# Kernel tuning notes

Hardware: AMD Instinct MI355X
Metric: run time of the kernel (lower is better)

## Reference

```python
import jax, jax.numpy as jnp
import numpy as np

N = 131072      # number of nodes / samples
IN_DIM = 128    # input_dim
H = 128         # hidden_dim
OUT_DIM = 10    # output_dim


def setup_inputs() -> dict:
    key = jax.random.key(0)
    ks = jax.random.split(key, 20)
    s = 0.05
    def rn(k, shape):
        return jax.random.normal(k, shape, jnp.float32) * s
    return {
        "x": jax.random.normal(ks[0], (N, IN_DIM), jnp.float32),
        # GRU layer 1 (seq_len=1, h0=0 => weight_hh contributes nothing; only b_hh matters)
        "w_ih_f1": rn(ks[1], (3 * H, IN_DIM)), "b_ih_f1": rn(ks[2], (3 * H,)), "b_hh_f1": rn(ks[3], (3 * H,)),
        "w_ih_b1": rn(ks[4], (3 * H, IN_DIM)), "b_ih_b1": rn(ks[5], (3 * H,)), "b_hh_b1": rn(ks[6], (3 * H,)),
        # GRU layer 2 (input 2H)
        "w_ih_f2": rn(ks[7], (3 * H, 2 * H)), "b_ih_f2": rn(ks[8], (3 * H,)), "b_hh_f2": rn(ks[9], (3 * H,)),
        "w_ih_b2": rn(ks[10], (3 * H, 2 * H)), "b_ih_b2": rn(ks[11], (3 * H,)), "b_hh_b2": rn(ks[12], (3 * H,)),
        # GCNConv layers
        "w_g1": rn(ks[13], (2 * H, 128)), "b_g1": rn(ks[14], (128,)),
        "w_g2": rn(ks[15], (128, 64)), "b_g2": rn(ks[16], (64,)),
        # final fc
        "w_fc": rn(ks[17], (64, OUT_DIM)), "b_fc": rn(ks[18], (OUT_DIM,)),
    }


def _gru_cell_zero(x, w_ih, b_ih, b_hh):
    # PyTorch GRU cell with h_prev = 0: h' = (1 - z) * n_gate
    gi = x @ w_ih.T + b_ih                    # [n, 3H]
    ir, iz, inn = jnp.split(gi, 3, axis=-1)
    hr, hz, hn = jnp.split(b_hh, 3)
    r = jax.nn.sigmoid(ir + hr)
    z = jax.nn.sigmoid(iz + hz)
    ng = jnp.tanh(inn + r * hn)
    return (1.0 - z) * ng


def _gcn(x, w, b, sources, targets, n):
    # PyG GCNConv: D^{-1/2}(A+I)D^{-1/2} X W + b, self-loops already in edge lists
    xw = x @ w                                 # [n, out]
    deg = jax.ops.segment_sum(jnp.ones(sources.shape[0], x.dtype), targets, num_segments=n)
    dinv = jax.lax.rsqrt(deg)
    norm = dinv[sources] * dinv[targets]       # [E]
    msg = norm[:, None] * xw[sources]          # gather
    return jax.ops.segment_sum(msg, targets, num_segments=n) + b  # scatter-add


def reference(x, w_ih_f1, b_ih_f1, b_hh_f1, w_ih_b1, b_ih_b1, b_hh_b1,
              w_ih_f2, b_ih_f2, b_hh_f2, w_ih_b2, b_ih_b2, b_hh_b2,
              w_g1, b_g1, w_g2, b_g2, w_fc, b_fc):
    n = x.shape[0]
    # seq_len = 1 => bidirectional GRU output is [fwd_cell(x); bwd_cell(x)]
    h1 = jnp.concatenate([_gru_cell_zero(x, w_ih_f1, b_ih_f1, b_hh_f1),
                          _gru_cell_zero(x, w_ih_b1, b_ih_b1, b_hh_b1)], axis=-1)
    h2 = jnp.concatenate([_gru_cell_zero(h1, w_ih_f2, b_ih_f2, b_hh_f2),
                          _gru_cell_zero(h1, w_ih_b2, b_ih_b2, b_hh_b2)], axis=-1)
    # chain graph, both directions, plus self loops (GCNConv adds them)
    src = jnp.arange(n - 1)
    dst = jnp.arange(1, n)
    ar = jnp.arange(n)
    sources = jnp.concatenate([src, dst, ar])
    targets = jnp.concatenate([dst, src, ar])
    g1 = _gcn(h2, w_g1, b_g1, sources, targets, n)   # dropout is identity in eval
    g2 = _gcn(g1, w_g2, b_g2, sources, targets, n)
    return g2 @ w_fc + b_fc
```

## Files before the change

kernel.cpp:

```cpp
#include <hip/hip_runtime.h>
#include <stdint.h>

#define N_NODES 131072
#define HDIM 128

typedef __bf16 bf16x8 __attribute__((ext_vector_type(8)));
typedef float f32x4 __attribute__((ext_vector_type(4)));
typedef unsigned short us8 __attribute__((ext_vector_type(8)));
typedef unsigned short ushort_t;

__device__ __forceinline__ float bf2f(ushort_t u) {
    union { float f; uint32_t i; } v; v.i = ((uint32_t)u) << 16; return v.f;
}
__device__ __forceinline__ ushort_t f2bf(float f) {
    union { float f; uint32_t i; } v; v.f = f;
    uint32_t i = v.i;
    return (ushort_t)((i + 0x7FFFu + ((i >> 16) & 1u)) >> 16);
}

__device__ __forceinline__ void gll16(const ushort_t* g, ushort_t* l) {
    __builtin_amdgcn_global_load_lds(
        (const __attribute__((address_space(1))) uint32_t*)g,
        (__attribute__((address_space(3))) uint32_t*)l, 16, 0, 0);
}

__device__ __forceinline__ bf16x8 ldsw(const ushort_t* base, int R, int g) {
    return *(const bf16x8*)&base[R * 64 + (((g - R) & 7) << 3)];
}

__device__ __forceinline__ float fsig(float x) {
    return __builtin_amdgcn_rcpf(1.0f + __expf(-x));
}
__device__ __forceinline__ float ftanh(float y) {
    float yc = fminf(fmaxf(y, -15.0f), 15.0f);
    float e = __expf(2.0f * yc);
    return (e - 1.0f) * __builtin_amdgcn_rcpf(e + 1.0f);
}

template<int NC>
__device__ __forceinline__ void swz(int b, int& m, int& c) {
    int mhi = b / (8 * NC);
    int rem = b - mhi * (8 * NC);
    c = rem >> 3;
    m = mhi * 8 + (rem & 7);
}

__global__ __launch_bounds__(256) void prep_weights(
    const float* __restrict__ w_f1, const float* __restrict__ w_b1,
    const float* __restrict__ w_f2, const float* __restrict__ w_b2,
    ushort_t* __restrict__ PWF1, ushort_t* __restrict__ PWB1,
    ushort_t* __restrict__ PWF2, ushort_t* __restrict__ PWB2)
{
    int idx = blockIdx.x * 256 + threadIdx.x;
    if (idx < 49152) {
        PWF1[idx] = f2bf(w_f1[idx]);
    } else if (idx < 98304) {
        int j = idx - 49152;  PWB1[j] = f2bf(w_b1[j]);
    } else if (idx < 196608) {
        int j = idx - 98304;  PWF2[j] = f2bf(w_f2[j]);
    } else if (idx < 294912) {
        int j = idx - 196608; PWB2[j] = f2bf(w_b2[j]);
    }
}

__global__ __launch_bounds__(256) void prep_M(
    const float* __restrict__ w_g1, const float* __restrict__ b_g1,
    const float* __restrict__ w_g2, const float* __restrict__ b_g2,
    const float* __restrict__ w_fc, const float* __restrict__ b_fc,
    ushort_t* __restrict__ M16, float* __restrict__ cc)
{
    __shared__ float wfc_s[640];
    __shared__ float T1[128][10];
    const int t = threadIdx.x;
    for (int i = t; i < 640; i += 256) wfc_s[i] = w_fc[i];
    __syncthreads();
    if (t < 128) {
        float s[10];
        #pragma unroll
        for (int j = 0; j < 10; ++j) s[j] = 0.0f;
        const float4* row = (const float4*)(w_g2 + t * 64);
        #pragma unroll
        for (int k4 = 0; k4 < 16; ++k4) {
            float4 v = row[k4];
            #pragma unroll
            for (int j = 0; j < 10; ++j)
                s[j] += v.x * wfc_s[(k4 * 4 + 0) * 10 + j] + v.y * wfc_s[(k4 * 4 + 1) * 10 + j]
                      + v.z * wfc_s[(k4 * 4 + 2) * 10 + j] + v.w * wfc_s[(k4 * 4 + 3) * 10 + j];
        }
        #pragma unroll
        for (int j = 0; j < 10; ++j) T1[t][j] = s[j];
    }
    __syncthreads();
    float m[10];
    #pragma unroll
    for (int j = 0; j < 10; ++j) m[j] = 0.0f;
    const float4* row1 = (const float4*)(w_g1 + t * 128);
    #pragma unroll 4
    for (int k4 = 0; k4 < 32; ++k4) {
        float4 v = row1[k4];
        #pragma unroll
        for (int j = 0; j < 10; ++j)
            m[j] += v.x * T1[k4 * 4 + 0][j] + v.y * T1[k4 * 4 + 1][j]
                  + v.z * T1[k4 * 4 + 2][j] + v.w * T1[k4 * 4 + 3][j];
    }
    #pragma unroll
    for (int j = 0; j < 16; ++j)
        M16[j * 256 + t] = (j < 10) ? f2bf(m[j]) : (ushort_t)0;
    if (t < 10) {
        float s1 = 0.0f;
        for (int k2 = 0; k2 < 128; ++k2) s1 += b_g1[k2] * T1[k2][t];
        cc[t] = s1;
        float s2 = 0.0f;
        for (int k3 = 0; k3 < 64; ++k3) s2 += b_g2[k3] * wfc_s[k3 * 10 + t];
        cc[16 + t] = s2 + b_fc[t];
    }
}

__global__ __launch_bounds__(256, 4) void gru_l1(
    const float* __restrict__ X,
    const ushort_t* __restrict__ Wf,
    const ushort_t* __restrict__ Wb,
    const float* __restrict__ bi_f, const float* __restrict__ bh_f,
    const float* __restrict__ bi_b, const float* __restrict__ bh_b,
    ushort_t* __restrict__ Hout)
{
    __shared__ ushort_t As[128 * 64];
    __shared__ ushort_t Bs[96 * 64];
    const int tid = threadIdx.x;
    int mt, comb;
    swz<8>(blockIdx.x, mt, comb);
    const int m0 = mt * 128;
    const int dir = comb >> 2;
    const int j0 = (comb & 3) * 32;
    const ushort_t* W = dir ? Wb : Wf;
    const float* b_ih = dir ? bi_b : bi_f;
    const float* b_hh = dir ? bh_b : bh_f;
    const int coloff = dir << 7;

    const int wv = tid >> 6, lane = tid & 63;
    const int lr = lane & 15, lq = lane >> 4;
    const int tr = tid >> 3, tc = tid & 7;
    const int sc = ((tr + tc) & 7) << 3;

    f32x4 acc[3][2][2];
    #pragma unroll
    for (int g = 0; g < 3; ++g)
        #pragma unroll
        for (int rt = 0; rt < 2; ++rt)
            #pragma unroll
            for (int ct = 0; ct < 2; ++ct)
                #pragma unroll
                for (int e = 0; e < 4; ++e) acc[g][rt][ct][e] = 0.0f;

    for (int t = 0; t < 2; ++t) {
        const int k0 = t * 64;
        const float* ga = X + (size_t)(m0 + tr) * 128 + k0 + sc;
        float4 fa[4][2];
        #pragma unroll
        for (int i = 0; i < 4; ++i) {
            const float4* p = (const float4*)(ga + (size_t)i * 32 * 128);
            fa[i][0] = p[0]; fa[i][1] = p[1];
        }
        #pragma unroll
        for (int i = 0; i < 3; ++i) {
            int wr = (i << 7) + j0 + tr;
            gll16(W + (size_t)wr * 128 + k0 + sc, &Bs[(i * 256 + tid) * 8]);
        }
        #pragma unroll
        for (int i = 0; i < 4; ++i) {
            us8 t8;
            t8[0] = f2bf(fa[i][0].x); t8[1] = f2bf(fa[i][0].y);
            t8[2] = f2bf(fa[i][0].z); t8[3] = f2bf(fa[i][0].w);
            t8[4] = f2bf(fa[i][1].x); t8[5] = f2bf(fa[i][1].y);
            t8[6] = f2bf(fa[i][1].z); t8[7] = f2bf(fa[i][1].w);
            *(us8*)&As[(i * 256 + tid) * 8] = t8;
        }
        __syncthreads();
        #pragma unroll
        for (int kk = 0; kk < 64; kk += 32) {
            const int g8 = (kk >> 3) + lq;
            bf16x8 a0 = ldsw(As, wv * 32 + lr, g8);
            bf16x8 a1 = ldsw(As, wv * 32 + 16 + lr, g8);
            #pragma unroll
            for (int g = 0; g < 3; ++g) {
                #pragma unroll
                for (int ct = 0; ct < 2; ++ct) {
                    bf16x8 b = ldsw(Bs, g * 32 + ct * 16 + lr, g8);
                    acc[g][0][ct] = __builtin_amdgcn_mfma_f32_16x16x32_bf16(a0, b, acc[g][0][ct], 0, 0, 0);
                    acc[g][1][ct] = __builtin_amdgcn_mfma_f32_16x16x32_bf16(a1, b, acc[g][1][ct], 0, 0, 0);
                }
            }
        }
        __syncthreads();
    }

    #pragma unroll
    for (int ct = 0; ct < 2; ++ct) {
        const int j = j0 + ct * 16 + lr;
        const float br  = b_ih[j] + b_hh[j];
        const float bz  = b_ih[HDIM + j] + b_hh[HDIM + j];
        const float bn  = b_ih[2 * HDIM + j];
        const float bhn = b_hh[2 * HDIM + j];
        #pragma unroll
        for (int rt = 0; rt < 2; ++rt) {
            #pragma unroll
            for (int r = 0; r < 4; ++r) {
                const int row = m0 + wv * 32 + rt * 16 + lq * 4 + r;
                float rg = fsig(acc[0][rt][ct][r] + br);
                float zg = fsig(acc[1][rt][ct][r] + bz);
                float ng = ftanh(acc[2][rt][ct][r] + bn + rg * bhn);
                Hout[(size_t)row * 256 + coloff + j] = f2bf((1.0f - zg) * ng);
            }
        }
    }
}

__global__ __launch_bounds__(256, 5) void gru_l2(
    const ushort_t* __restrict__ A,
    const ushort_t* __restrict__ Wf,
    const ushort_t* __restrict__ Wb,
    const float* __restrict__ bi_f, const float* __restrict__ bh_f,
    const float* __restrict__ bi_b, const float* __restrict__ bh_b,
    const ushort_t* __restrict__ M16,
    float* __restrict__ Zp)
{
    __shared__ ushort_t As[128 * 64];
    __shared__ ushort_t Bs[96 * 64];
    const int tid = threadIdx.x;
    int mt, comb;
    swz<8>(blockIdx.x, mt, comb);
    const int m0 = mt * 128;
    const int dir = comb >> 2;
    const int j0 = (comb & 3) * 32;
    const ushort_t* W = dir ? Wb : Wf;
    const float* b_ih = dir ? bi_b : bi_f;
    const float* b_hh = dir ? bh_b : bh_f;
    const int coloff = dir << 7;

    const int wv = tid >> 6, lane = tid & 63;
    const int lr = lane & 15, lq = lane >> 4;
    const int tr = tid >> 3, tc = tid & 7;
    const int sc = ((tr + tc) & 7) << 3;

    f32x4 acc[3][2][2];
    #pragma unroll
    for (int g = 0; g < 3; ++g)
        #pragma unroll
        for (int rt = 0; rt < 2; ++rt)
            #pragma unroll
            for (int ct = 0; ct < 2; ++ct)
                #pragma unroll
                for (int e = 0; e < 4; ++e) acc[g][rt][ct][e] = 0.0f;

    for (int t = 0; t < 4; ++t) {
        const int k0 = t * 64;
        const ushort_t* ga = A + (size_t)(m0 + tr) * 256 + k0 + sc;
        #pragma unroll
        for (int i = 0; i < 4; ++i)
            gll16(ga + (size_t)i * 32 * 256, &As[(i * 256 + tid) * 8]);
        #pragma unroll
        for (int i = 0; i < 3; ++i) {
            int wr = (i << 7) + j0 + tr;
            gll16(W + (size_t)wr * 256 + k0 + sc, &Bs[(i * 256 + tid) * 8]);
        }
        __syncthreads();
        #pragma unroll
        for (int kk = 0; kk < 64; kk += 32) {
            const int g8 = (kk >> 3) + lq;
            bf16x8 a0 = ldsw(As, wv * 32 + lr, g8);
            bf16x8 a1 = ldsw(As, wv * 32 + 16 + lr, g8);
            #pragma unroll
            for (int g = 0; g < 3; ++g) {
                #pragma unroll
                for (int ct = 0; ct < 2; ++ct) {
                    bf16x8 b = ldsw(Bs, g * 32 + ct * 16 + lr, g8);
                    acc[g][0][ct] = __builtin_amdgcn_mfma_f32_16x16x32_bf16(a0, b, acc[g][0][ct], 0, 0, 0);
                    acc[g][1][ct] = __builtin_amdgcn_mfma_f32_16x16x32_bf16(a1, b, acc[g][1][ct], 0, 0, 0);
                }
            }
        }
        __syncthreads();
    }

    const bf16x8 mb = *(const bf16x8*)&M16[lr * 256 + coloff + j0 + lq * 8];

    ushort_t* hs = &As[wv * 1280];
    #pragma unroll
    for (int ct = 0; ct < 2; ++ct) {
        const int j = j0 + ct * 16 + lr;
        const float br  = b_ih[j] + b_hh[j];
        const float bz  = b_ih[HDIM + j] + b_hh[HDIM + j];
        const float bn  = b_ih[2 * HDIM + j];
        const float bhn = b_hh[2 * HDIM + j];
        #pragma unroll
        for (int rt = 0; rt < 2; ++rt) {
            #pragma unroll
            for (int r = 0; r < 4; ++r) {
                const int lrow = rt * 16 + lq * 4 + r;
                float rg = fsig(acc[0][rt][ct][r] + br);
                float zg = fsig(acc[1][rt][ct][r] + bz);
                float ng = ftanh(acc[2][rt][ct][r] + bn + rg * bhn);
                hs[lrow * 40 + ct * 16 + lr] = f2bf((1.0f - zg) * ng);
            }
        }
    }
    __syncthreads();

    bf16x8 ha0 = *(const bf16x8*)&hs[lr * 40 + lq * 8];
    bf16x8 ha1 = *(const bf16x8*)&hs[(16 + lr) * 40 + lq * 8];
    f32x4 z0, z1;
    #pragma unroll
    for (int e = 0; e < 4; ++e) { z0[e] = 0.0f; z1[e] = 0.0f; }
    z0 = __builtin_amdgcn_mfma_f32_16x16x32_bf16(ha0, mb, z0, 0, 0, 0);
    z1 = __builtin_amdgcn_mfma_f32_16x16x32_bf16(ha1, mb, z1, 0, 0, 0);

    if (lr < 10) {
        float* zslice = Zp + (size_t)comb * (N_NODES * 10);
        #pragma unroll
        for (int r = 0; r < 4; ++r) {
            zslice[(size_t)(m0 + wv * 32 + lq * 4 + r) * 10 + lr] = z0[r];
            zslice[(size_t)(m0 + wv * 32 + 16 + lq * 4 + r) * 10 + lr] = z1[r];
        }
    }
}

__global__ __launch_bounds__(256) void zsum(
    const float4* __restrict__ Zp4, float4* __restrict__ Zc4)
{
    int i = blockIdx.x * 256 + threadIdx.x;
    float4 a = Zp4[i];
    #pragma unroll
    for (int s = 1; s < 8; ++s) {
        float4 b = Zp4[(size_t)s * 327680 + i];
        a.x += b.x; a.y += b.y; a.z += b.z; a.w += b.w;
    }
    Zc4[i] = a;
}

__device__ __forceinline__ float dcoef(int i) {
    return (i == 0 || i == N_NODES - 1) ? 0.70710678118654752f : 0.57735026918962576f;
}
__global__ __launch_bounds__(256) void st5(
    const float* __restrict__ z, float* __restrict__ out,
    const float* __restrict__ cc)
{
    int idx = blockIdx.x * 256 + threadIdx.x;
    int i = idx >> 4, c = idx & 15;
    if (c >= 10) return;
    float d_i = dcoef(i);
    float accv = 0.0f, dsum = d_i;
    #pragma unroll
    for (int oj = -1; oj <= 1; ++oj) {
        int j = i + oj;
        if (j < 0 || j >= N_NODES) continue;
        float dj = dcoef(j);
        if (oj != 0) dsum += dj;
        float wj = 0.0f;
        #pragma unroll
        for (int ok = -1; ok <= 1; ++ok) {
            int k = j + ok;
            if (k < 0 || k >= N_NODES) continue;
            wj += dcoef(k) * z[(size_t)k * 10 + c];
        }
        accv += dj * dj * wj;
    }
    out[(size_t)i * 10 + c] = d_i * accv + d_i * dsum * cc[c] + cc[16 + c];
}

extern "C" void kernel_launch(void* const* d_in, const int* in_sizes, int n_in,
                              void* d_out, int out_size, void* d_ws, size_t ws_size,
                              hipStream_t stream) {
    const float* x     = (const float*)d_in[0];
    const float* w_f1  = (const float*)d_in[1];
    const float* bi_f1 = (const float*)d_in[2];
    const float* bh_f1 = (const float*)d_in[3];
    const float* w_b1  = (const float*)d_in[4];
    const float* bi_b1 = (const float*)d_in[5];
    const float* bh_b1 = (const float*)d_in[6];
    const float* w_f2  = (const float*)d_in[7];
    const float* bi_f2 = (const float*)d_in[8];
    const float* bh_f2 = (const float*)d_in[9];
    const float* w_b2  = (const float*)d_in[10];
    const float* bi_b2 = (const float*)d_in[11];
    const float* bh_b2 = (const float*)d_in[12];
    const float* w_g1  = (const float*)d_in[13];
    const float* b_g1  = (const float*)d_in[14];
    const float* w_g2  = (const float*)d_in[15];
    const float* b_g2  = (const float*)d_in[16];
    const float* w_fc  = (const float*)d_in[17];
    const float* b_fc  = (const float*)d_in[18];

    char* ws = (char*)d_ws;
    ushort_t* h1   = (ushort_t*)(ws);
    float*    Zp   = (float*)(ws + 67108864);
    float*    Zc   = (float*)(ws + 109051904);
    ushort_t* PWF1 = (ushort_t*)(ws + 134217728);
    ushort_t* PWB1 = PWF1 + 49152;
    ushort_t* PWF2 = PWB1 + 49152;
    ushort_t* PWB2 = PWF2 + 98304;
    ushort_t* M16  = PWB2 + 98304;
    float*    cc   = (float*)(M16 + 4096);

    prep_weights<<<1152, 256, 0, stream>>>(w_f1, w_b1, w_f2, w_b2,
                                           PWF1, PWB1, PWF2, PWB2);
    prep_M<<<1, 256, 0, stream>>>(w_g1, b_g1, w_g2, b_g2, w_fc, b_fc, M16, cc);

    gru_l1<<<N_NODES / 128 * 8, 256, 0, stream>>>(
        x, PWF1, PWB1, bi_f1, bh_f1, bi_b1, bh_b1, h1);
    gru_l2<<<N_NODES / 128 * 8, 256, 0, stream>>>(
        h1, PWF2, PWB2, bi_f2, bh_f2, bi_b2, bh_b2, M16, Zp);

    zsum<<<1280, 256, 0, stream>>>((const float4*)Zp, (float4*)Zc);
    st5<<<N_NODES * 16 / 256, 256, 0, stream>>>(Zc, (float*)d_out, cc);
}
```

Measured before the change: 278.1 us.

## Fuse prep kernels, fold partial-sum reduction into stencil, use native bf16 casts

Merges the two weight-prep kernels into one launch by having the last block compute the fused GCN/FC matrix. Removes the separate zsum kernel: the stencil kernel now sums the 8 partial Z slices for its 5 neighbours directly, saving a launch and a write/read of the reduced buffer but re-reading each partial value up to five times. Replaces the manual round-to-nearest bf16 conversion with native __bf16 casts, which can map to hardware convert instructions. Raises the gru_l1 occupancy hint from 4 to 5 waves per SIMD, which may force register spilling.

```diff
diff --git a/kernel.cpp b/kernel.cpp
--- a/kernel.cpp
+++ b/kernel.cpp
@@ -45,25 +45,11 @@
     m = mhi * 8 + (rem & 7);
 }
 
-__global__ __launch_bounds__(256) void prep_weights(
+__global__ __launch_bounds__(256) void prep_all(
     const float* __restrict__ w_f1, const float* __restrict__ w_b1,
     const float* __restrict__ w_f2, const float* __restrict__ w_b2,
     ushort_t* __restrict__ PWF1, ushort_t* __restrict__ PWB1,
-    ushort_t* __restrict__ PWF2, ushort_t* __restrict__ PWB2)
-{
-    int idx = blockIdx.x * 256 + threadIdx.x;
-    if (idx < 49152) {
-        PWF1[idx] = f2bf(w_f1[idx]);
-    } else if (idx < 98304) {
-        int j = idx - 49152;  PWB1[j] = f2bf(w_b1[j]);
-    } else if (idx < 196608) {
-        int j = idx - 98304;  PWF2[j] = f2bf(w_f2[j]);
-    } else if (idx < 294912) {
-        int j = idx - 196608; PWB2[j] = f2bf(w_b2[j]);
-    }
-}
-
-__global__ __launch_bounds__(256) void prep_M(
+    ushort_t* __restrict__ PWF2, ushort_t* __restrict__ PWB2,
     const float* __restrict__ w_g1, const float* __restrict__ b_g1,
     const float* __restrict__ w_g2, const float* __restrict__ b_g2,
     const float* __restrict__ w_fc, const float* __restrict__ b_fc,
@@ -72,6 +58,21 @@
     __shared__ float wfc_s[640];
     __shared__ float T1[128][10];
     const int t = threadIdx.x;
+
+    if (blockIdx.x < 1152) {
+        int idx = blockIdx.x * 256 + t;
+        if (idx < 49152) {
+            PWF1[idx] = f2bf(w_f1[idx]);
+        } else if (idx < 98304) {
+            int j = idx - 49152;  PWB1[j] = f2bf(w_b1[j]);
+        } else if (idx < 196608) {
+            int j = idx - 98304;  PWF2[j] = f2bf(w_f2[j]);
+        } else if (idx < 294912) {
+            int j = idx - 196608; PWB2[j] = f2bf(w_b2[j]);
+        }
+        return;
+    }
+
     for (int i = t; i < 640; i += 256) wfc_s[i] = w_fc[i];
     __syncthreads();
     if (t < 128) {
@@ -116,7 +117,7 @@
     }
 }
 
-__global__ __launch_bounds__(256, 4) void gru_l1(
+__global__ __launch_bounds__(256, 5) void gru_l1(
     const float* __restrict__ X,
     const ushort_t* __restrict__ Wf,
     const ushort_t* __restrict__ Wb,
@@ -168,12 +169,12 @@
         }
         #pragma unroll
         for (int i = 0; i < 4; ++i) {
-            us8 t8;
-            t8[0] = f2bf(fa[i][0].x); t8[1] = f2bf(fa[i][0].y);
-            t8[2] = f2bf(fa[i][0].z); t8[3] = f2bf(fa[i][0].w);
-            t8[4] = f2bf(fa[i][1].x); t8[5] = f2bf(fa[i][1].y);
-            t8[6] = f2bf(fa[i][1].z); t8[7] = f2bf(fa[i][1].w);
-            *(us8*)&As[(i * 256 + tid) * 8] = t8;
+            bf16x8 t8;
+            t8[0] = (__bf16)fa[i][0].x; t8[1] = (__bf16)fa[i][0].y;
+            t8[2] = (__bf16)fa[i][0].z; t8[3] = (__bf16)fa[i][0].w;
+            t8[4] = (__bf16)fa[i][1].x; t8[5] = (__bf16)fa[i][1].y;
+            t8[6] = (__bf16)fa[i][1].z; t8[7] = (__bf16)fa[i][1].w;
+            *(bf16x8*)&As[(i * 256 + tid) * 8] = t8;
         }
         __syncthreads();
         #pragma unroll
@@ -209,7 +210,7 @@
                 float rg = fsig(acc[0][rt][ct][r] + br);
                 float zg = fsig(acc[1][rt][ct][r] + bz);
                 float ng = ftanh(acc[2][rt][ct][r] + bn + rg * bhn);
-                Hout[(size_t)row * 256 + coloff + j] = f2bf((1.0f - zg) * ng);
+                ((__bf16*)Hout)[(size_t)row * 256 + coloff + j] = (__bf16)((1.0f - zg) * ng);
             }
         }
     }
@@ -300,7 +301,7 @@
                 float rg = fsig(acc[0][rt][ct][r] + br);
                 float zg = fsig(acc[1][rt][ct][r] + bz);
                 float ng = ftanh(acc[2][rt][ct][r] + bn + rg * bhn);
-                hs[lrow * 40 + ct * 16 + lr] = f2bf((1.0f - zg) * ng);
+                ((__bf16*)hs)[lrow * 40 + ct * 16 + lr] = (__bf16)((1.0f - zg) * ng);
             }
         }
     }
@@ -324,29 +325,30 @@
     }
 }
 
-__global__ __launch_bounds__(256) void zsum(
-    const float4* __restrict__ Zp4, float4* __restrict__ Zc4)
-{
-    int i = blockIdx.x * 256 + threadIdx.x;
-    float4 a = Zp4[i];
-    #pragma unroll
-    for (int s = 1; s < 8; ++s) {
-        float4 b = Zp4[(size_t)s * 327680 + i];
-        a.x += b.x; a.y += b.y; a.z += b.z; a.w += b.w;
-    }
-    Zc4[i] = a;
-}
-
 __device__ __forceinline__ float dcoef(int i) {
     return (i == 0 || i == N_NODES - 1) ? 0.70710678118654752f : 0.57735026918962576f;
 }
 __global__ __launch_bounds__(256) void st5(
-    const float* __restrict__ z, float* __restrict__ out,
+    const float* __restrict__ Zp, float* __restrict__ out,
     const float* __restrict__ cc)
 {
     int idx = blockIdx.x * 256 + threadIdx.x;
     int i = idx >> 4, c = idx & 15;
     if (c >= 10) return;
+
+    float zk[5];
+    #pragma unroll
+    for (int o = 0; o < 5; ++o) {
+        int k = i + o - 2;
+        float v = 0.0f;
+        if (k >= 0 && k < N_NODES) {
+            #pragma unroll
+            for (int s = 0; s < 8; ++s)
+                v += Zp[(size_t)s * ((size_t)N_NODES * 10) + (size_t)k * 10 + c];
+        }
+        zk[o] = v;
+    }
+
     float d_i = dcoef(i);
     float accv = 0.0f, dsum = d_i;
     #pragma unroll
@@ -360,7 +362,7 @@
         for (int ok = -1; ok <= 1; ++ok) {
             int k = j + ok;
             if (k < 0 || k >= N_NODES) continue;
-            wj += dcoef(k) * z[(size_t)k * 10 + c];
+            wj += dcoef(k) * zk[k - i + 2];
         }
         accv += dj * dj * wj;
     }
@@ -393,7 +395,6 @@
     char* ws = (char*)d_ws;
     ushort_t* h1   = (ushort_t*)(ws);
     float*    Zp   = (float*)(ws + 67108864);
-    float*    Zc   = (float*)(ws + 109051904);
     ushort_t* PWF1 = (ushort_t*)(ws + 134217728);
     ushort_t* PWB1 = PWF1 + 49152;
     ushort_t* PWF2 = PWB1 + 49152;
@@ -401,15 +402,15 @@
     ushort_t* M16  = PWB2 + 98304;
     float*    cc   = (float*)(M16 + 4096);
 
-    prep_weights<<<1152, 256, 0, stream>>>(w_f1, w_b1, w_f2, w_b2,
-                                           PWF1, PWB1, PWF2, PWB2);
-    prep_M<<<1, 256, 0, stream>>>(w_g1, b_g1, w_g2, b_g2, w_fc, b_fc, M16, cc);
+    prep_all<<<1153, 256, 0, stream>>>(w_f1, w_b1, w_f2, w_b2,
+                                       PWF1, PWB1, PWF2, PWB2,
+                                       w_g1, b_g1, w_g2, b_g2, w_fc, b_fc,
+                                       M16, cc);
 
     gru_l1<<<N_NODES / 128 * 8, 256, 0, stream>>>(
         x, PWF1, PWB1, bi_f1, bh_f1, bi_b1, bh_b1, h1);
     gru_l2<<<N_NODES / 128 * 8, 256, 0, stream>>>(
         h1, PWF2, PWB2, bi_f2, bh_f2, bi_b2, bh_b2, M16, Zp);
 
-    zsum<<<1280, 256, 0, stream>>>((const float4*)Zp, (float4*)Zc);
-    st5<<<N_NODES * 16 / 256, 256, 0, stream>>>(Zc, (float*)d_out, cc);
-}
+    st5<<<N_NODES * 16 / 256, 256, 0, stream>>>(Zp, (float*)d_out, cc);
+}
```

Measured after the change: 286.5 us. +3.0%, slower.
